# Kernel optimization log

Hardware: AMD Instinct MI355X
Metric: run time of the kernel (lower is better)

Reference implementation:

```python
import jax, jax.numpy as jnp
import numpy as np

B, N, D, H = 128, 2000, 128, 8
HD = D // H  # head_dim = 16
CLIP = 10.0


def setup_inputs() -> dict:
    key = jax.random.key(0)
    ks = jax.random.split(key, 20)
    s = 0.05
    w = lambda k, sh: jax.random.normal(k, sh, jnp.float32) * s
    return {
        "embeddings": jax.random.normal(ks[0], (B, N, D), jnp.float32),
        "context": jax.random.normal(ks[1], (B, D), jnp.float32),
        "step_context": jax.random.normal(ks[2], (B, 1, D + 1), jnp.float32),
        "mask": jax.random.randint(ks[3], (B, 1, N), 0, 2).astype(bool),
        "Wq_c": w(ks[4], (D, D)), "bq_c": w(ks[5], (D,)),
        "Wq_s": w(ks[6], (D, D + 1)), "bq_s": w(ks[7], (D,)),
        "Wk": w(ks[8], (D, D)), "bk": w(ks[9], (D,)),
        "Wkt": w(ks[10], (D, D)), "bkt": w(ks[11], (D,)),
        "Wv": w(ks[12], (D, D)), "bv": w(ks[13], (D,)),
        "Wo": w(ks[14], (D, D)), "bo": w(ks[15], (D,)),
    }


def _heads(x):
    # (B, S, D) -> (B, H, S, HD)
    return x.reshape(x.shape[0], x.shape[1], H, HD).transpose(0, 2, 1, 3)


def reference(embeddings, context, step_context, mask,
              Wq_c, bq_c, Wq_s, bq_s, Wk, bk, Wkt, bkt, Wv, bv, Wo, bo):
    # get_projections
    K = _heads(embeddings @ Wk.T + bk)        # (B, H, N, HD)
    V = _heads(embeddings @ Wv.T + bv)        # (B, H, N, HD)
    K_tanh = embeddings @ Wkt.T + bkt         # (B, N, D)
    Q_context = context[:, None, :] @ Wq_c.T + bq_c     # (B, 1, D)
    Q_step = step_context @ Wq_s.T + bq_s                # (B, 1, D)
    Q = _heads(Q_context + Q_step)            # (B, H, 1, HD)

    # decoder_mha: matmul -> mask(-inf) -> softmax -> mask(0) -> matmul -> w_out
    compat = jnp.einsum('bhqd,bhkd->bhqk', Q, K) / jnp.sqrt(jnp.float32(HD))
    m4 = mask[:, None, :, :]                  # (B, 1, 1, N) broadcast over heads
    compat = jnp.where(m4, -jnp.inf, compat)
    attn_w = jax.nn.softmax(compat, axis=-1)
    attn_w = jnp.where(m4, 0.0, attn_w)
    attn = jnp.einsum('bhqk,bhkd->bhqd', attn_w, V)      # (B, H, 1, HD)
    mha = attn.transpose(0, 2, 1, 3).reshape(B, -1, D) @ Wo.T + bo  # (B, 1, D)

    # get_log_p: matmul -> mask(-inf) -> log_softmax
    # NOTE: the original computes tanh(compat)*clip into `x` but never uses it
    # (dead code) -- replicated faithfully by omitting the clip.
    logits = jnp.einsum('bqd,bkd->bqk', mha, K_tanh) / jnp.sqrt(jnp.float32(D))
    logits = jnp.where(mask, -jnp.inf, logits)
    return jax.nn.log_softmax(logits, axis=-1)  # (B, 1, N)
```

## Files before the change

### kernel.cpp

```cpp
#include <hip/hip_runtime.h>
#include <cstdint>
#include <cstddef>
#include <math.h>

#define B 128
#define N 2000
#define D 128
#define H 8
#define HD 16
#define NC 8
#define TPC 250
#define NEG_BIG (-1.0e30f)

__global__ __launch_bounds__(128) void k_prep(
    const float* __restrict__ ctx, const float* __restrict__ sctx,
    const float* __restrict__ Wq_c, const float* __restrict__ bq_c,
    const float* __restrict__ Wq_s, const float* __restrict__ bq_s,
    const float* __restrict__ Wk,   const float* __restrict__ bk,
    float* __restrict__ wq, float* __restrict__ cq)
{
    int b = blockIdx.x, t = threadIdx.x;
    __shared__ float4 c14[D / 4];
    __shared__ float c2s[D + 1], Qs[D];
    if (t < D / 4) c14[t] = reinterpret_cast<const float4*>(ctx + b * D)[t];
    c2s[t] = sctx[b * (D + 1) + t];
    if (t == 0) c2s[D] = sctx[b * (D + 1) + D];
    __syncthreads();
    float q = bq_c[t] + bq_s[t];
    const float4* wc4 = reinterpret_cast<const float4*>(Wq_c + t * D);
    #pragma unroll 8
    for (int j = 0; j < D / 4; j++) {
        float4 w = wc4[j], c = c14[j];
        q += w.x * c.x + w.y * c.y + w.z * c.z + w.w * c.w;
    }
    const float* wsr = Wq_s + t * (D + 1);
    #pragma unroll 8
    for (int j = 0; j < D + 1; j++) q += wsr[j] * c2s[j];
    Qs[t] = q;
    __syncthreads();
    float acc[H] = {};
    #pragma unroll
    for (int r = 0; r < D; r++)
        acc[r >> 4] += Wk[r * D + t] * Qs[r];
    #pragma unroll
    for (int h = 0; h < H; h++) wq[b * (H * D) + h * D + t] = acc[h] * 0.25f;
    if (t < H) {
        float c = 0.f;
        #pragma unroll
        for (int i = 0; i < HD; i++) c += Qs[t * HD + i] * bk[t * HD + i];
        cq[b * H + t] = c * 0.25f;
    }
}

__global__ __launch_bounds__(256) void k_attn(
    const float* __restrict__ emb, const unsigned char* __restrict__ mask,
    const float* __restrict__ wq, const float* __restrict__ cq,
    float* __restrict__ pm, float* __restrict__ pl, float* __restrict__ ps)
{
    int b = blockIdx.y, c = blockIdx.x, t = threadIdx.x;
    int n0 = c * TPC;

    __shared__ float4 wqs[H][D / 4];
    __shared__ float  cqs[H];
    __shared__ float  plds[H][256];
    __shared__ float  redf[4][H];
    __shared__ float4 reds[4][H][D / 4];

    wqs[t >> 5][t & 31] = reinterpret_cast<const float4*>(wq + b * (H * D))[t];
    if (t < H) cqs[t] = cq[b * H + t];
    __syncthreads();

    int  tt   = (t < TPC) ? t : (TPC - 1);
    int  n    = n0 + tt;
    bool dead = (t >= TPC) || (mask[b * N + n] != 0);
    float cval[H];
    {
        const float4* e4 = reinterpret_cast<const float4*>(emb + ((size_t)b * N + n) * D);
        float acc[H] = {};
        #pragma unroll 4
        for (int d4 = 0; d4 < D / 4; d4++) {
            float4 e = e4[d4];
            #pragma unroll
            for (int h = 0; h < H; h++) {
                float4 w = wqs[h][d4];
                acc[h] += e.x * w.x + e.y * w.y + e.z * w.z + e.w * w.w;
            }
        }
        #pragma unroll
        for (int h = 0; h < H; h++)
            cval[h] = dead ? -INFINITY : (acc[h] + cqs[h]);
    }

    float mx[H];
    #pragma unroll
    for (int h = 0; h < H; h++) mx[h] = cval[h];
    #pragma unroll
    for (int o = 32; o; o >>= 1)
        #pragma unroll
        for (int h = 0; h < H; h++) mx[h] = fmaxf(mx[h], __shfl_xor(mx[h], o));
    if ((t & 63) == 0)
        #pragma unroll
        for (int h = 0; h < H; h++) redf[t >> 6][h] = mx[h];
    __syncthreads();
    float mfin[H];
    #pragma unroll
    for (int h = 0; h < H; h++)
        mfin[h] = fmaxf(fmaxf(redf[0][h], redf[1][h]), fmaxf(redf[2][h], redf[3][h]));
    __syncthreads();

    float ls[H];
    #pragma unroll
    for (int h = 0; h < H; h++) {
        float p = (cval[h] == -INFINITY) ? 0.f : __expf(cval[h] - mfin[h]);
        plds[h][t] = p;
        ls[h] = p;
    }
    #pragma unroll
    for (int o = 32; o; o >>= 1)
        #pragma unroll
        for (int h = 0; h < H; h++) ls[h] += __shfl_xor(ls[h], o);
    if ((t & 63) == 0)
        #pragma unroll
        for (int h = 0; h < H; h++) redf[t >> 6][h] = ls[h];
    __syncthreads();
    if (t < H) {
        float l = redf[0][t] + redf[1][t] + redf[2][t] + redf[3][t];
        pm[(b * NC + c) * H + t] = mfin[t];
        pl[(b * NC + c) * H + t] = l;
    }

    int d4 = t & 31, tg = t >> 5;
    const float4* e4 = reinterpret_cast<const float4*>(emb + (size_t)b * N * D) + d4;
    float4 a[H];
    #pragma unroll
    for (int h = 0; h < H; h++) a[h] = {0.f, 0.f, 0.f, 0.f};
    for (int i = tg; i < TPC; i += 8) {
        float4 e = e4[(size_t)(n0 + i) * (D / 4)];
        #pragma unroll
        for (int h = 0; h < H; h++) {
            float w = plds[h][i];
            a[h].x += w * e.x; a[h].y += w * e.y;
            a[h].z += w * e.z; a[h].w += w * e.w;
        }
    }
    #pragma unroll
    for (int h = 0; h < H; h++) {
        a[h].x += __shfl_xor(a[h].x, 32);
        a[h].y += __shfl_xor(a[h].y, 32);
        a[h].z += __shfl_xor(a[h].z, 32);
        a[h].w += __shfl_xor(a[h].w, 32);
    }
    if ((t & 32) == 0) {
        int wave = t >> 6;
        #pragma unroll
        for (int h = 0; h < H; h++) reds[wave][h][d4] = a[h];
    }
    __syncthreads();
    int hh = t >> 5, dd = t & 31;
    float4 r = reds[0][hh][dd];
    #pragma unroll
    for (int g2 = 1; g2 < 4; g2++) {
        float4 x = reds[g2][hh][dd];
        r.x += x.x; r.y += x.y; r.z += x.z; r.w += x.w;
    }
    reinterpret_cast<float4*>(ps + (((size_t)(b * NC + c)) * H + hh) * D)[dd] = r;
}

__global__ __launch_bounds__(128) void k_comb(
    const float* __restrict__ pm, const float* __restrict__ pl, const float* __restrict__ ps,
    const float* __restrict__ Wv, const float* __restrict__ bv,
    const float* __restrict__ Wo, const float* __restrict__ bo,
    const float* __restrict__ Wkt, const float* __restrict__ bkt,
    float* __restrict__ g, float* __restrict__ c2)
{
    int b = blockIdx.x, t = threadIdx.x;
    __shared__ float scale[NC][H];
    __shared__ float s_s[H][D + 4];
    __shared__ float attn_s[D];
    __shared__ float mha_s[D];
    if (t < H) {
        float M = -INFINITY;
        #pragma unroll
        for (int c = 0; c < NC; c++) M = fmaxf(M, pm[(b * NC + c) * H + t]);
        float L = 0.f;
        float e[NC];
        #pragma unroll
        for (int c = 0; c < NC; c++) {
            float m = pm[(b * NC + c) * H + t];
            e[c] = (m == -INFINITY) ? 0.f : __expf(m - M);
            L += pl[(b * NC + c) * H + t] * e[c];
        }
        float invL = 1.0f / L;
        #pragma unroll
        for (int c = 0; c < NC; c++) scale[c][t] = e[c] * invL;
    }
    __syncthreads();
    #pragma unroll
    for (int h = 0; h < H; h++) {
        float v = 0.f;
        #pragma unroll
        for (int c = 0; c < NC; c++)
            v += ps[(((size_t)(b * NC + c)) * H + h) * D + t] * scale[c][h];
        s_s[h][t] = v;
    }
    __syncthreads();
    {
        int h = t >> 4;
        const float* wr = Wv + t * D;
        float a = bv[t];
        #pragma unroll 8
        for (int d = 0; d < D; d++) a += wr[d] * s_s[h][d];
        attn_s[t] = a;
    }
    __syncthreads();
    {
        const float* wr = Wo + t * D;
        float m = bo[t];
        #pragma unroll 8
        for (int r = 0; r < D; r++) m += wr[r] * attn_s[r];
        mha_s[t] = m;
    }
    __syncthreads();
    {
        float gv = 0.f;
        #pragma unroll 8
        for (int d = 0; d < D; d++) gv += Wkt[d * D + t] * mha_s[d];
        g[b * D + t] = gv * 0.08838834764831845f;
    }
    if (t == 0) {
        float c = 0.f;
        #pragma unroll 8
        for (int d = 0; d < D; d++) c += mha_s[d] * bkt[d];
        c2[b] = c * 0.08838834764831845f;
    }
}

__global__ __launch_bounds__(256) void k_logits(
    const float* __restrict__ emb, const unsigned char* __restrict__ mask,
    const float* __restrict__ g, const float* __restrict__ c2,
    float* __restrict__ out)
{
    int b = blockIdx.y;
    int t = threadIdx.x;
    int n = blockIdx.x * 256 + t;
    __shared__ float4 gs[D / 4];
    __shared__ float c2s;
    if (t < D / 4) gs[t] = reinterpret_cast<const float4*>(g + b * D)[t];
    if (t == 0) c2s = c2[b];
    __syncthreads();
    if (n >= N) return;
    const float4* e4 = reinterpret_cast<const float4*>(emb + ((size_t)b * N + n) * D);
    float a0 = 0.f, a1 = 0.f;
    #pragma unroll 4
    for (int d4 = 0; d4 < D / 4; d4 += 2) {
        float4 e = e4[d4],     w = gs[d4];
        float4 f = e4[d4 + 1], x = gs[d4 + 1];
        a0 += e.x * w.x + e.y * w.y + e.z * w.z + e.w * w.w;
        a1 += f.x * x.x + f.y * x.y + f.z * x.z + f.w * x.w;
    }
    bool m = mask[b * N + n] != 0;
    out[(size_t)b * N + n] = m ? -INFINITY : (a0 + a1 + c2s);
}

__global__ __launch_bounds__(256) void k_lsm(float* __restrict__ out)
{
    __shared__ float red[4];
    int t = threadIdx.x;
    float* row = out + (size_t)blockIdx.x * N;
    float v[8];
    float mx = -INFINITY;
    #pragma unroll
    for (int i = 0; i < 8; i++) {
        int idx = t + i * 256;
        v[i] = (idx < N) ? row[idx] : -INFINITY;
        mx = fmaxf(mx, v[i]);
    }
    #pragma unroll
    for (int o = 32; o; o >>= 1) mx = fmaxf(mx, __shfl_xor(mx, o));
    if ((t & 63) == 0) red[t >> 6] = mx;
    __syncthreads();
    mx = fmaxf(fmaxf(red[0], red[1]), fmaxf(red[2], red[3]));
    __syncthreads();
    float s = 0.f;
    #pragma unroll
    for (int i = 0; i < 8; i++)
        if (v[i] != -INFINITY) s += __expf(v[i] - mx);
    #pragma unroll
    for (int o = 32; o; o >>= 1) s += __shfl_xor(s, o);
    if ((t & 63) == 0) red[t >> 6] = s;
    __syncthreads();
    s = red[0] + red[1] + red[2] + red[3];
    float lse = mx + logf(s);
    #pragma unroll
    for (int i = 0; i < 8; i++) {
        int idx = t + i * 256;
        if (idx < N) row[idx] = (v[i] == -INFINITY) ? NEG_BIG : (v[i] - lse);
    }
}

extern "C" void kernel_launch(void* const* d_in, const int* in_sizes, int n_in,
                              void* d_out, int out_size, void* d_ws, size_t ws_size,
                              hipStream_t stream)
{
    const float* emb  = (const float*)d_in[0];
    const float* ctx  = (const float*)d_in[1];
    const float* sctx = (const float*)d_in[2];
    const unsigned char* mask = (const unsigned char*)d_in[3];
    const float* Wq_c = (const float*)d_in[4];
    const float* bq_c = (const float*)d_in[5];
    const float* Wq_s = (const float*)d_in[6];
    const float* bq_s = (const float*)d_in[7];
    const float* Wk   = (const float*)d_in[8];
    const float* bk   = (const float*)d_in[9];
    const float* Wkt  = (const float*)d_in[10];
    const float* bkt  = (const float*)d_in[11];
    const float* Wv   = (const float*)d_in[12];
    const float* bv   = (const float*)d_in[13];
    const float* Wo   = (const float*)d_in[14];
    const float* bo   = (const float*)d_in[15];
    float* out = (float*)d_out;

    float* ws = (float*)d_ws;
    float* wq = ws;
    float* cq = ws + 131072;
    float* pm = ws + 132096;
    float* pl = ws + 140288;
    float* ps = ws + 148480;
    float* g  = ws + 1197056;
    float* c2 = ws + 1213440;

    k_prep  <<<dim3(B), dim3(128), 0, stream>>>(ctx, sctx, Wq_c, bq_c, Wq_s, bq_s, Wk, bk, wq, cq);
    k_attn  <<<dim3(NC, B), dim3(256), 0, stream>>>(emb, mask, wq, cq, pm, pl, ps);
    k_comb  <<<dim3(B), dim3(128), 0, stream>>>(pm, pl, ps, Wv, bv, Wo, bo, Wkt, bkt, g, c2);
    k_logits<<<dim3((N + 255) / 256, B), dim3(256), 0, stream>>>(emb, mask, g, c2, out);
    k_lsm   <<<dim3(B), dim3(256), 0, stream>>>(out);
}
```

Baseline: 107.1 us.

## Use quad-per-token coalesced embedding reads with online softmax in attention and logits

Measured after the change: 114.9 us, median of 2. 1.07x slower.

```diff
diff --git a/kernel.cpp b/kernel.cpp
--- a/kernel.cpp
+++ b/kernel.cpp
@@ -10,6 +10,8 @@
 #define HD 16
 #define NC 8
 #define TPC 250
+#define SC 64
+#define NIT 4
 #define NEG_BIG (-1.0e30f)
 
 __global__ __launch_bounds__(128) void k_prep(
@@ -59,90 +61,109 @@
 {
     int b = blockIdx.y, c = blockIdx.x, t = threadIdx.x;
     int n0 = c * TPC;
-
-    __shared__ float4 wqs[H][D / 4];
+    int lane = t & 63, wave = t >> 6;
+    int qtok = t >> 2, qp = t & 3;
+    int grp = t >> 5, gl = t & 31;
+
+    __shared__ float4 wqs[H][32];
     __shared__ float  cqs[H];
-    __shared__ float  plds[H][256];
-    __shared__ float  redf[4][H];
-    __shared__ float4 reds[4][H][D / 4];
+    __shared__ float  plds[H][SC];
+    __shared__ float  redm[4][H], redl[4][H];
+    __shared__ float4 reds[4][H][32];
 
     wqs[t >> 5][t & 31] = reinterpret_cast<const float4*>(wq + b * (H * D))[t];
     if (t < H) cqs[t] = cq[b * H + t];
     __syncthreads();
 
-    int  tt   = (t < TPC) ? t : (TPC - 1);
-    int  n    = n0 + tt;
-    bool dead = (t >= TPC) || (mask[b * N + n] != 0);
-    float cval[H];
-    {
-        const float4* e4 = reinterpret_cast<const float4*>(emb + ((size_t)b * N + n) * D);
+    float M[H], L[H];
+    float4 a[H];
+    #pragma unroll
+    for (int h = 0; h < H; h++) { M[h] = -INFINITY; L[h] = 0.f; a[h] = {0.f, 0.f, 0.f, 0.f}; }
+
+    const float4* e4 = reinterpret_cast<const float4*>(emb + (size_t)b * N * D);
+
+    for (int it = 0; it < NIT; it++) {
+        int base = it * SC;
+        int ng = base + qtok;
+        bool live = (ng < TPC);
+        int nr = live ? (n0 + ng) : n0;
+        bool dead = !live || (mask[(size_t)b * N + nr] != 0);
+
         float acc[H] = {};
-        #pragma unroll 4
-        for (int d4 = 0; d4 < D / 4; d4++) {
-            float4 e = e4[d4];
+        const float4* erow = e4 + (size_t)nr * 32;
+        #pragma unroll
+        for (int j = 0; j < 8; j++) {
+            float4 e = erow[j * 4 + qp];
             #pragma unroll
             for (int h = 0; h < H; h++) {
-                float4 w = wqs[h][d4];
+                float4 w = wqs[h][j * 4 + qp];
                 acc[h] += e.x * w.x + e.y * w.y + e.z * w.z + e.w * w.w;
             }
         }
-        #pragma unroll
-        for (int h = 0; h < H; h++)
-            cval[h] = dead ? -INFINITY : (acc[h] + cqs[h]);
-    }
-
-    float mx[H];
-    #pragma unroll
-    for (int h = 0; h < H; h++) mx[h] = cval[h];
-    #pragma unroll
-    for (int o = 32; o; o >>= 1)
-        #pragma unroll
-        for (int h = 0; h < H; h++) mx[h] = fmaxf(mx[h], __shfl_xor(mx[h], o));
-    if ((t & 63) == 0)
-        #pragma unroll
-        for (int h = 0; h < H; h++) redf[t >> 6][h] = mx[h];
-    __syncthreads();
-    float mfin[H];
-    #pragma unroll
-    for (int h = 0; h < H; h++)
-        mfin[h] = fmaxf(fmaxf(redf[0][h], redf[1][h]), fmaxf(redf[2][h], redf[3][h]));
-    __syncthreads();
-
-    float ls[H];
-    #pragma unroll
-    for (int h = 0; h < H; h++) {
-        float p = (cval[h] == -INFINITY) ? 0.f : __expf(cval[h] - mfin[h]);
-        plds[h][t] = p;
-        ls[h] = p;
-    }
-    #pragma unroll
-    for (int o = 32; o; o >>= 1)
-        #pragma unroll
-        for (int h = 0; h < H; h++) ls[h] += __shfl_xor(ls[h], o);
-    if ((t & 63) == 0)
-        #pragma unroll
-        for (int h = 0; h < H; h++) redf[t >> 6][h] = ls[h];
-    __syncthreads();
-    if (t < H) {
-        float l = redf[0][t] + redf[1][t] + redf[2][t] + redf[3][t];
-        pm[(b * NC + c) * H + t] = mfin[t];
-        pl[(b * NC + c) * H + t] = l;
-    }
-
-    int d4 = t & 31, tg = t >> 5;
-    const float4* e4 = reinterpret_cast<const float4*>(emb + (size_t)b * N * D) + d4;
-    float4 a[H];
-    #pragma unroll
-    for (int h = 0; h < H; h++) a[h] = {0.f, 0.f, 0.f, 0.f};
-    for (int i = tg; i < TPC; i += 8) {
-        float4 e = e4[(size_t)(n0 + i) * (D / 4)];
-        #pragma unroll
-        for (int h = 0; h < H; h++) {
-            float w = plds[h][i];
-            a[h].x += w * e.x; a[h].y += w * e.y;
-            a[h].z += w * e.z; a[h].w += w * e.w;
-        }
-    }
+        float cv[H];
+        #pragma unroll
+        for (int h = 0; h < H; h++) {
+            float v = acc[h];
+            v += __shfl_xor(v, 1);
+            v += __shfl_xor(v, 2);
+            cv[h] = dead ? -INFINITY : (v + cqs[h]);
+        }
+
+        float mx[H];
+        #pragma unroll
+        for (int h = 0; h < H; h++) mx[h] = cv[h];
+        #pragma unroll
+        for (int o = 4; o <= 32; o <<= 1)
+            #pragma unroll
+            for (int h = 0; h < H; h++) mx[h] = fmaxf(mx[h], __shfl_xor(mx[h], o));
+        if (lane == 0)
+            #pragma unroll
+            for (int h = 0; h < H; h++) redm[wave][h] = mx[h];
+        __syncthreads();
+        float Mn[H], sc_[H];
+        #pragma unroll
+        for (int h = 0; h < H; h++) {
+            float m2 = fmaxf(fmaxf(redm[0][h], redm[1][h]), fmaxf(redm[2][h], redm[3][h]));
+            Mn[h] = fmaxf(M[h], m2);
+            sc_[h] = (M[h] == -INFINITY) ? 0.f : __expf(M[h] - Mn[h]);
+        }
+
+        float sp[H];
+        #pragma unroll
+        for (int h = 0; h < H; h++) {
+            float p = (cv[h] == -INFINITY) ? 0.f : __expf(cv[h] - Mn[h]);
+            if (qp == 0) plds[h][qtok] = p;
+            sp[h] = p;
+        }
+        #pragma unroll
+        for (int o = 4; o <= 32; o <<= 1)
+            #pragma unroll
+            for (int h = 0; h < H; h++) sp[h] += __shfl_xor(sp[h], o);
+        if (lane == 0)
+            #pragma unroll
+            for (int h = 0; h < H; h++) redl[wave][h] = sp[h];
+        __syncthreads();
+        #pragma unroll
+        for (int h = 0; h < H; h++) {
+            float lc = redl[0][h] + redl[1][h] + redl[2][h] + redl[3][h];
+            L[h] = L[h] * sc_[h] + lc;
+            M[h] = Mn[h];
+            a[h].x *= sc_[h]; a[h].y *= sc_[h]; a[h].z *= sc_[h]; a[h].w *= sc_[h];
+        }
+
+        int lim = (TPC - base < SC) ? (TPC - base) : SC;
+        for (int i = grp; i < lim; i += 8) {
+            float4 e = e4[(size_t)(n0 + base + i) * 32 + gl];
+            #pragma unroll
+            for (int h = 0; h < H; h++) {
+                float w = plds[h][i];
+                a[h].x += w * e.x; a[h].y += w * e.y;
+                a[h].z += w * e.z; a[h].w += w * e.w;
+            }
+        }
+        __syncthreads();
+    }
+
     #pragma unroll
     for (int h = 0; h < H; h++) {
         a[h].x += __shfl_xor(a[h].x, 32);
@@ -150,20 +171,27 @@
         a[h].z += __shfl_xor(a[h].z, 32);
         a[h].w += __shfl_xor(a[h].w, 32);
     }
-    if ((t & 32) == 0) {
-        int wave = t >> 6;
-        #pragma unroll
-        for (int h = 0; h < H; h++) reds[wave][h][d4] = a[h];
-    }
-    __syncthreads();
-    int hh = t >> 5, dd = t & 31;
-    float4 r = reds[0][hh][dd];
-    #pragma unroll
-    for (int g2 = 1; g2 < 4; g2++) {
-        float4 x = reds[g2][hh][dd];
-        r.x += x.x; r.y += x.y; r.z += x.z; r.w += x.w;
-    }
-    reinterpret_cast<float4*>(ps + (((size_t)(b * NC + c)) * H + hh) * D)[dd] = r;
+    if ((t & 32) == 0)
+        #pragma unroll
+        for (int h = 0; h < H; h++) reds[wave][h][gl] = a[h];
+    __syncthreads();
+    {
+        int hh = t >> 5, dd = t & 31;
+        float4 r = reds[0][hh][dd];
+        #pragma unroll
+        for (int w2 = 1; w2 < 4; w2++) {
+            float4 x = reds[w2][hh][dd];
+            r.x += x.x; r.y += x.y; r.z += x.z; r.w += x.w;
+        }
+        reinterpret_cast<float4*>(ps + (((size_t)(b * NC + c)) * H + hh) * D)[dd] = r;
+    }
+    if (t == 0) {
+        #pragma unroll
+        for (int h = 0; h < H; h++) {
+            pm[(b * NC + c) * H + h] = M[h];
+            pl[(b * NC + c) * H + h] = L[h];
+        }
+    }
 }
 
 __global__ __launch_bounds__(128) void k_comb(
@@ -240,26 +268,34 @@
     const float* __restrict__ g, const float* __restrict__ c2,
     float* __restrict__ out)
 {
-    int b = blockIdx.y;
-    int t = threadIdx.x;
-    int n = blockIdx.x * 256 + t;
+    int b = blockIdx.y, t = threadIdx.x;
+    int qtok = t >> 2, qp = t & 3;
     __shared__ float4 gs[D / 4];
     __shared__ float c2s;
     if (t < D / 4) gs[t] = reinterpret_cast<const float4*>(g + b * D)[t];
     if (t == 0) c2s = c2[b];
     __syncthreads();
-    if (n >= N) return;
-    const float4* e4 = reinterpret_cast<const float4*>(emb + ((size_t)b * N + n) * D);
-    float a0 = 0.f, a1 = 0.f;
-    #pragma unroll 4
-    for (int d4 = 0; d4 < D / 4; d4 += 2) {
-        float4 e = e4[d4],     w = gs[d4];
-        float4 f = e4[d4 + 1], x = gs[d4 + 1];
-        a0 += e.x * w.x + e.y * w.y + e.z * w.z + e.w * w.w;
-        a1 += f.x * x.x + f.y * x.y + f.z * x.z + f.w * x.w;
-    }
-    bool m = mask[b * N + n] != 0;
-    out[(size_t)b * N + n] = m ? -INFINITY : (a0 + a1 + c2s);
+    int n0 = blockIdx.x * TPC;
+    const float4* e4 = reinterpret_cast<const float4*>(emb + (size_t)b * N * D);
+    for (int k = 0; k < NIT; k++) {
+        int ng = k * SC + qtok;
+        bool live = (ng < TPC);
+        int nr = live ? (n0 + ng) : n0;
+        const float4* erow = e4 + (size_t)nr * 32;
+        float acc = 0.f;
+        #pragma unroll
+        for (int j = 0; j < 8; j++) {
+            float4 e = erow[j * 4 + qp];
+            float4 w = gs[j * 4 + qp];
+            acc += e.x * w.x + e.y * w.y + e.z * w.z + e.w * w.w;
+        }
+        acc += __shfl_xor(acc, 1);
+        acc += __shfl_xor(acc, 2);
+        if (live && qp == 0) {
+            bool m = mask[(size_t)b * N + nr] != 0;
+            out[(size_t)b * N + nr] = m ? -INFINITY : (acc + c2s);
+        }
+    }
 }
 
 __global__ __launch_bounds__(256) void k_lsm(float* __restrict__ out)
@@ -332,6 +368,6 @@
     k_prep  <<<dim3(B), dim3(128), 0, stream>>>(ctx, sctx, Wq_c, bq_c, Wq_s, bq_s, Wk, bk, wq, cq);
     k_attn  <<<dim3(NC, B), dim3(256), 0, stream>>>(emb, mask, wq, cq, pm, pl, ps);
     k_comb  <<<dim3(B), dim3(128), 0, stream>>>(pm, pl, ps, Wv, bv, Wo, bo, Wkt, bkt, g, c2);
-    k_logits<<<dim3((N + 255) / 256, B), dim3(256), 0, stream>>>(emb, mask, g, c2, out);
+    k_logits<<<dim3(NC, B), dim3(256), 0, stream>>>(emb, mask, g, c2, out);
     k_lsm   <<<dim3(B), dim3(256), 0, stream>>>(out);
 }
```
